# Optimization experiments

Measured on AMD Instinct MI355X. Metric: run time of the kernel, lower is better.

## Reference

```python
import jax, jax.numpy as jnp
import numpy as np
from jax import lax

LEAK = 0.2
GN_EPS = 1e-5
K_NEIGH = 16
GROUPS = 4


def knn_idx(coor_k, coor_q, k):
    # coor_k: [B,Nk,3], coor_q: [B,Nq,3] -> [B,Nq,k] indices of k nearest in coor_k
    d = (jnp.sum(coor_q * coor_q, -1, keepdims=True)
         - 2.0 * jnp.einsum('bqc,bkc->bqk', coor_q, coor_k)
         + jnp.sum(coor_k * coor_k, -1)[:, None, :])
    _, idx = lax.top_k(-d, k)
    return idx


def graph_feature(coor_q, x_q, coor_k, x_k, k):
    # coor_*: [B,3,N*]; x_q: [B,C,Nq]; x_k: [B,C,Nk] -> [B,2C,Nq,k]
    idx = knn_idx(lax.stop_gradient(coor_k).transpose(0, 2, 1),
                  lax.stop_gradient(coor_q).transpose(0, 2, 1), k)
    B = x_k.shape[0]
    x_k_t = x_k.transpose(0, 2, 1)                      # [B,Nk,C]
    b_idx = jnp.arange(B)[:, None, None]
    nb = x_k_t[b_idx, idx]                              # [B,Nq,k,C]
    nb = nb.transpose(0, 3, 1, 2)                       # [B,C,Nq,k]
    xq = x_q[:, :, :, None]                             # [B,C,Nq,1]
    return jnp.concatenate([nb - xq, jnp.broadcast_to(xq, nb.shape)], axis=1)


def conv_gn_lrelu_max(f, w, gamma, beta):
    # f: [B,Cin,N,k]; w: [Cout,Cin] -> [B,Cout,N] (max over k)
    y = jnp.einsum('oc,bcnk->bonk', w, f)
    B, C, N, Kk = y.shape
    g = y.reshape(B, GROUPS, C // GROUPS, N, Kk)
    mu = g.mean((2, 3, 4), keepdims=True)
    var = g.var((2, 3, 4), keepdims=True)
    g = (g - mu) * lax.rsqrt(var + GN_EPS)
    y = g.reshape(B, C, N, Kk) * gamma[None, :, None, None] + beta[None, :, None, None]
    y = jnp.where(y >= 0, y, LEAK * y)
    return y.max(axis=-1)


def fps(xyz, n):
    # xyz: [B,N,3] -> [B,n] int32 (furthest point sampling, start at index 0)
    B, N, _ = xyz.shape
    d0 = jnp.sum((xyz - xyz[:, :1]) ** 2, -1)           # dist to point 0
    def body(dist, _):
        idx = jnp.argmax(dist, -1)                       # [B]
        nxt = jnp.take_along_axis(xyz, idx[:, None, None], 1)
        dist = jnp.minimum(dist, jnp.sum((xyz - nxt) ** 2, -1))
        return dist, idx
    _, idxs = lax.scan(body, d0, None, length=n - 1)     # [n-1,B]
    first = jnp.zeros((1, B), idxs.dtype)
    return jnp.concatenate([first, idxs], 0).T           # [B,n]


def fps_downsample(coor, x, n):
    # coor: [B,3,N], x: [B,C,N] -> ([B,3,n], [B,C,n])
    idx = fps(lax.stop_gradient(coor).transpose(0, 2, 1), n)
    comb = jnp.concatenate([coor, x], axis=1)            # [B,3+C,N]
    b_idx = jnp.arange(coor.shape[0])[:, None]
    new = comb.transpose(0, 2, 1)[b_idx, idx].transpose(0, 2, 1)
    return new[:, :3], new[:, 3:]


def setup_inputs() -> dict:
    key = jax.random.key(0)
    ks = jax.random.split(key, 16)
    s = 0.1
    return {
        'x': jax.random.normal(ks[0], (32, 2048, 3), jnp.float32),
        'w_in': jax.random.normal(ks[1], (8, 3), jnp.float32) * s,
        'b_in': jnp.zeros((8,), jnp.float32),
        'w1': jax.random.normal(ks[2], (32, 16), jnp.float32) * s,
        'g1': jnp.ones((32,), jnp.float32), 'be1': jnp.zeros((32,), jnp.float32),
        'w2': jax.random.normal(ks[3], (64, 64), jnp.float32) * s,
        'g2': jnp.ones((64,), jnp.float32), 'be2': jnp.zeros((64,), jnp.float32),
        'w3': jax.random.normal(ks[4], (64, 128), jnp.float32) * s,
        'g3': jnp.ones((64,), jnp.float32), 'be3': jnp.zeros((64,), jnp.float32),
        'w4': jax.random.normal(ks[5], (256, 128), jnp.float32) * s,
        'g4': jnp.ones((256,), jnp.float32), 'be4': jnp.zeros((256,), jnp.float32),
        'num0': 512,
        'num1': 128,
    }


def reference(x, w_in, b_in, w1, g1, be1, w2, g2, be2, w3, g3, be3, w4, g4, be4, num0, num1):
    coor = x.transpose(0, 2, 1)                          # [B,3,N]
    f = jnp.einsum('oc,bcn->bon', w_in, coor) + b_in[None, :, None]  # input_trans
    f = graph_feature(coor, f, coor, f, K_NEIGH)         # [B,16,N,k]
    f = conv_gn_lrelu_max(f, w1, g1, be1)                # [B,32,N]
    coor_q, f_q = fps_downsample(coor, f, num0)
    f = graph_feature(coor_q, f_q, coor, f, K_NEIGH)     # [B,64,num0,k]
    f = conv_gn_lrelu_max(f, w2, g2, be2)                # [B,64,num0]
    coor = coor_q
    f = graph_feature(coor, f, coor, f, K_NEIGH)         # [B,128,num0,k]
    f = conv_gn_lrelu_max(f, w3, g3, be3)                # [B,64,num0]
    coor_q, f_q = fps_downsample(coor, f, num1)
    f = graph_feature(coor_q, f_q, coor, f, K_NEIGH)     # [B,128,num1,k]
    f = conv_gn_lrelu_max(f, w4, g4, be4)                # [B,256,num1]
    coor = coor_q
    return coor.transpose(0, 2, 1), f.transpose(0, 2, 1)  # [B,num1,3], [B,num1,256]
```

## Files before the change

kernel.cpp:

```cpp
#include <hip/hip_runtime.h>

#define BB 32
#define NPTS0 2048
#define KNB 16
#define KC 256

constexpr int ilog2c(int n){ int l=0; while(n>1){ n>>=1; ++l; } return l; }

static __device__ __forceinline__ float sq3(float a, float b, float c){
  return __fadd_rn(__fadd_rn(__fmul_rn(a,a),__fmul_rn(b,b)),__fmul_rn(c,c));
}

template<int CTRL, int RM>
static __device__ __forceinline__ float dpp_maxf(float v){
  int s = __builtin_amdgcn_update_dpp(__float_as_int(v), __float_as_int(v), CTRL, RM, 0xF, false);
  return fmaxf(v, __int_as_float(s));
}
template<int CTRL, int RM>
static __device__ __forceinline__ unsigned dpp_minu(unsigned v){
  unsigned s = (unsigned)__builtin_amdgcn_update_dpp((int)v, (int)v, CTRL, RM, 0xF, false);
  return s < v ? s : v;
}

static __device__ __forceinline__ void proj_body(const float* __restrict__ x,
    const float* __restrict__ w, const float* __restrict__ bias, float* __restrict__ f0,
    int blk)
{
  int gid = blk*256 + threadIdx.x;
  if (gid >= BB*NPTS0) return;
  float x0 = x[gid*3+0], x1 = x[gid*3+1], x2 = x[gid*3+2];
  #pragma unroll
  for (int o = 0; o < 8; ++o){
    float acc = __fmul_rn(w[o*3+0], x0);
    acc = __fmaf_rn(w[o*3+1], x1, acc);
    acc = __fmaf_rn(w[o*3+2], x2, acc);
    f0[gid*8+o] = __fadd_rn(acc, bias[o]);
  }
}

#define KDECL(I) float th##I = __builtin_inff(); int ti##I = 0;
#define KINS(I,J) if (th##I < th##J){ float tv=th##I; th##I=th##J; th##J=tv; \
                                      int tj=ti##I; ti##I=ti##J; ti##J=tj; }
#define KST(I) pd[base+I] = th##I; pi[base+I] = (unsigned char)ti##I;

static __device__ __forceinline__ void knn_part_body(const float* __restrict__ qpts,
    const float* __restrict__ kpts, int Nq, int Nk, int nkc,
    float* __restrict__ pd, unsigned char* __restrict__ pi,
    int b, int qcb, int kc, float4* kk4)
{
  int tid = threadIdx.x;
  {
    int j = kc*KC + tid;
    float a = kpts[(b*Nk+j)*3+0];
    float c = kpts[(b*Nk+j)*3+1];
    float d = kpts[(b*Nk+j)*3+2];
    kk4[tid] = make_float4(a, c, d, sq3(a,c,d));
  }
  __syncthreads();
  int q = qcb*256 + tid;
  if (q >= Nq) return;
  float qx = qpts[(b*Nq+q)*3+0], qy = qpts[(b*Nq+q)*3+1], qz = qpts[(b*Nq+q)*3+2];
  float qq = sq3(qx,qy,qz);
  KDECL(0) KDECL(1) KDECL(2) KDECL(3) KDECL(4) KDECL(5) KDECL(6) KDECL(7)
  KDECL(8) KDECL(9) KDECL(10) KDECL(11) KDECL(12) KDECL(13) KDECL(14) KDECL(15)
  for (int j=0;j<KC;j++){
    float4 k4 = kk4[j];
    float dot = __fmul_rn(qx,k4.x);
    dot = __fmaf_rn(qy,k4.y,dot);
    dot = __fmaf_rn(qz,k4.z,dot);
    float d = __fadd_rn(__fsub_rn(qq, __fmul_rn(2.0f,dot)), k4.w);
    if (d < th15){
      th15 = d; ti15 = j;
      KINS(15,14) KINS(14,13) KINS(13,12) KINS(12,11) KINS(11,10) KINS(10,9)
      KINS(9,8) KINS(8,7) KINS(7,6) KINS(6,5) KINS(5,4) KINS(4,3) KINS(3,2)
      KINS(2,1) KINS(1,0)
    }
  }
  size_t base = ((size_t)(b*Nq+q)*nkc + kc)*KNB;
  KST(0) KST(1) KST(2) KST(3) KST(4) KST(5) KST(6) KST(7)
  KST(8) KST(9) KST(10) KST(11) KST(12) KST(13) KST(14) KST(15)
}

#define FPS_LOAD(T) float px##T, py##T, pz##T, d##T; { int i_=T*256+tid; \
  px##T=P[i_*3+0]; py##T=P[i_*3+1]; pz##T=P[i_*3+2]; \
  float dx_=__fsub_rn(px##T,c0x), dy_=__fsub_rn(py##T,c0y), dz_=__fsub_rn(pz##T,c0z); \
  d##T=sq3(dx_,dy_,dz_); bm=fmaxf(bm,d##T); }
#define FPS_MATCH(T) if (d##T == m_w) ci = (unsigned)(T*256 + tid);
#define FPS_OWN(T) if ((idx_w>>8) == T##u){ cx=px##T; cy=py##T; cz=pz##T; }
#define FPS_UPD(T) { float dx_=__fsub_rn(px##T,sx), dy_=__fsub_rn(py##T,sy), dz_=__fsub_rn(pz##T,sz); \
  float nd_=sq3(dx_,dy_,dz_); d##T=fminf(d##T,nd_); nbm=fmaxf(nbm,d##T); }

#define FPS_REDUCE_AND_PICK \
    float v = bm; \
    v = dpp_maxf<0x111, 0xF>(v); \
    v = dpp_maxf<0x112, 0xF>(v); \
    v = dpp_maxf<0x114, 0xF>(v); \
    v = dpp_maxf<0x118, 0xF>(v); \
    v = dpp_maxf<0x142, 0xA>(v); \
    v = dpp_maxf<0x143, 0xC>(v); \
    float m_w = __int_as_float(__builtin_amdgcn_readlane(__float_as_int(v), 63)); \
    unsigned ci = 0xFFFFFFFFu;

#define FPS_MIN_AND_MERGE \
    ci = dpp_minu<0x111, 0xF>(ci); \
    ci = dpp_minu<0x112, 0xF>(ci); \
    ci = dpp_minu<0x114, 0xF>(ci); \
    ci = dpp_minu<0x118, 0xF>(ci); \
    ci = dpp_minu<0x142, 0xA>(ci); \
    ci = dpp_minu<0x143, 0xC>(ci); \
    unsigned idx_w = (unsigned)__builtin_amdgcn_readlane((int)ci, 63); \
    int par = s & 1;

#define FPS_CROSSWAVE \
    __syncthreads(); \
    float4 q0 = *(const float4*)&swp[par][0][0]; float z0 = swp[par][0][4]; \
    float4 q1 = *(const float4*)&swp[par][1][0]; float z1 = swp[par][1][4]; \
    float4 q2 = *(const float4*)&swp[par][2][0]; float z2 = swp[par][2][4]; \
    float4 q3 = *(const float4*)&swp[par][3][0]; float z3 = swp[par][3][4]; \
    float mm = q0.x; unsigned mi = __float_as_uint(q0.y); \
    float sx = q0.z, sy = q0.w, sz = z0; \
    if (q1.x > mm || (q1.x == mm && __float_as_uint(q1.y) < mi)){ \
      mm = q1.x; mi = __float_as_uint(q1.y); sx = q1.z; sy = q1.w; sz = z1; } \
    if (q2.x > mm || (q2.x == mm && __float_as_uint(q2.y) < mi)){ \
      mm = q2.x; mi = __float_as_uint(q2.y); sx = q2.z; sy = q2.w; sz = z2; } \
    if (q3.x > mm || (q3.x == mm && __float_as_uint(q3.y) < mi)){ \
      mm = q3.x; mi = __float_as_uint(q3.y); sx = q3.z; sy = q3.w; sz = z3; } \
    if (tid == 0) oibuf[s] = (int)mi;

static __device__ __forceinline__ void fps8_body(const float* __restrict__ pts,
    int S, int* __restrict__ oidx, int b, char* smraw)
{
  float (*swp)[4][8] = reinterpret_cast<float(*)[4][8]>(smraw);
  int* oibuf = reinterpret_cast<int*>(smraw + 256);
  int tid = threadIdx.x, wid = tid >> 6;
  const float* P = pts + (size_t)b*2048*3;
  float c0x = P[0], c0y = P[1], c0z = P[2];
  float bm = -1.0f;
  FPS_LOAD(0) FPS_LOAD(1) FPS_LOAD(2) FPS_LOAD(3)
  FPS_LOAD(4) FPS_LOAD(5) FPS_LOAD(6) FPS_LOAD(7)
  if (tid == 0) oibuf[0] = 0;
  for (int s=1; s<S; ++s){
    FPS_REDUCE_AND_PICK
    FPS_MATCH(7) FPS_MATCH(6) FPS_MATCH(5) FPS_MATCH(4)
    FPS_MATCH(3) FPS_MATCH(2) FPS_MATCH(1) FPS_MATCH(0)
    FPS_MIN_AND_MERGE
    if (tid == (int)(idx_w & 255u)){
      float cx = px0, cy = py0, cz = pz0;
      FPS_OWN(1) FPS_OWN(2) FPS_OWN(3) FPS_OWN(4) FPS_OWN(5) FPS_OWN(6) FPS_OWN(7)
      float4* wp = (float4*)&swp[par][wid][0];
      *wp = make_float4(m_w, __uint_as_float(idx_w), cx, cy);
      swp[par][wid][4] = cz;
    }
    FPS_CROSSWAVE
    float nbm = -1.0f;
    FPS_UPD(0) FPS_UPD(1) FPS_UPD(2) FPS_UPD(3)
    FPS_UPD(4) FPS_UPD(5) FPS_UPD(6) FPS_UPD(7)
    bm = nbm;
  }
  __syncthreads();
  for (int s2 = tid; s2 < S; s2 += 256) oidx[b*S + s2] = oibuf[s2];
}

static __device__ __forceinline__ void fps2_body(const float* __restrict__ pts,
    int S, int* __restrict__ oidx, int b, char* smraw)
{
  float (*swp)[4][8] = reinterpret_cast<float(*)[4][8]>(smraw);
  int* oibuf = reinterpret_cast<int*>(smraw + 256);
  int tid = threadIdx.x, wid = tid >> 6;
  const float* P = pts + (size_t)b*512*3;
  float c0x = P[0], c0y = P[1], c0z = P[2];
  float bm = -1.0f;
  FPS_LOAD(0) FPS_LOAD(1)
  if (tid == 0) oibuf[0] = 0;
  for (int s=1; s<S; ++s){
    FPS_REDUCE_AND_PICK
    FPS_MATCH(1) FPS_MATCH(0)
    FPS_MIN_AND_MERGE
    if (tid == (int)(idx_w & 255u)){
      float cx = px0, cy = py0, cz = pz0;
      FPS_OWN(1)
      float4* wp = (float4*)&swp[par][wid][0];
      *wp = make_float4(m_w, __uint_as_float(idx_w), cx, cy);
      swp[par][wid][4] = cz;
    }
    FPS_CROSSWAVE
    float nbm = -1.0f;
    FPS_UPD(0) FPS_UPD(1)
    bm = nbm;
  }
  __syncthreads();
  for (int s2 = tid; s2 < S; s2 += 256) oidx[b*S + s2] = oibuf[s2];
}

__global__ __launch_bounds__(256) void fused1_kernel(const float* __restrict__ x,
    const float* __restrict__ w_in, const float* __restrict__ b_in,
    float* __restrict__ f0, float* __restrict__ pd1, unsigned char* __restrict__ pi1,
    int* __restrict__ fidx0)
{
  __shared__ __align__(16) char sm[4096];
  int bid = blockIdx.x;
  if (bid < 32){
    __builtin_amdgcn_s_setprio(3);
    fps8_body(x, 512, fidx0, bid, sm);
  } else if (bid < 32+2048){
    int r = bid - 32;
    int b = r & 31; int rest = r >> 5;
    knn_part_body(x, x, 2048, 2048, 8, pd1, pi1, b, rest & 7, rest >> 3, (float4*)sm);
  } else {
    proj_body(x, w_in, b_in, f0, bid - 2080);
  }
}

__global__ __launch_bounds__(256) void fused2_kernel(const float* __restrict__ coorq1,
    const float* __restrict__ x,
    float* __restrict__ pd2, unsigned char* __restrict__ pi2,
    float* __restrict__ pd3, unsigned char* __restrict__ pi3,
    int* __restrict__ fidx1)
{
  __shared__ __align__(16) char sm[4096];
  int bid = blockIdx.x;
  if (bid < 32){
    __builtin_amdgcn_s_setprio(3);
    fps2_body(coorq1, 128, fidx1, bid, sm);
  } else if (bid < 32+512){
    int r = bid - 32;
    int b = r & 31; int rest = r >> 5;
    knn_part_body(coorq1, x, 512, 2048, 8, pd2, pi2, b, rest & 1, rest >> 1, (float4*)sm);
  } else {
    int r = bid - 544;
    int b = r & 31; int rest = r >> 5;
    knn_part_body(coorq1, coorq1, 512, 512, 2, pd3, pi3, b, rest & 1, rest >> 1, (float4*)sm);
  }
}

__global__ __launch_bounds__(256) void knn_part_kernel(const float* __restrict__ qpts,
    const float* __restrict__ kpts, int Nq, int Nk,
    float* __restrict__ pd, unsigned char* __restrict__ pi)
{
  __shared__ __align__(16) float4 kk4[KC];
  knn_part_body(qpts, kpts, Nq, Nk, gridDim.z, pd, pi,
                blockIdx.x, blockIdx.y, blockIdx.z, kk4);
}

__global__ __launch_bounds__(256) void knn_merge_kernel(const float* __restrict__ pd,
    const unsigned char* __restrict__ pi, int Nq, int nkc, int* __restrict__ oidx)
{
  int gid = blockIdx.x*256 + threadIdx.x;
  if (gid >= BB*Nq) return;
  float th[KNB]; int ti[KNB];
  #pragma unroll
  for (int i=0;i<KNB;i++){ th[i] = __builtin_inff(); ti[i] = 0; }
  size_t base = (size_t)gid*nkc*KNB;
  for (int kc=0;kc<nkc;kc++){
    size_t cb = base + (size_t)kc*KNB;
    for (int i=0;i<KNB;i++){
      float d = pd[cb+i];
      if (d >= th[KNB-1]) break;
      int j = kc*KC + (int)pi[cb+i];
      th[KNB-1] = d; ti[KNB-1] = j;
      #pragma unroll
      for (int m=KNB-1;m>0;--m){
        if (th[m] < th[m-1]){
          float tv=th[m]; th[m]=th[m-1]; th[m-1]=tv;
          int tj=ti[m]; ti[m]=ti[m-1]; ti[m-1]=tj;
        }
      }
    }
  }
  #pragma unroll
  for (int i=0;i<KNB;i++) oidx[gid*KNB + i] = ti[i];
}

template<int C, int O, bool DIFF>
__global__ __launch_bounds__(256) void gemv_kernel(const float* __restrict__ fin,
    const float* __restrict__ W, float* __restrict__ out, int Npts)
{
  constexpr int NT = O/8;
  constexpr int LNT = ilog2c(NT);
  int gid = blockIdx.x*256 + threadIdx.x;
  if (gid >= BB*Npts*NT) return;
  int tile = gid & (NT-1);
  int pn = gid >> LNT;
  const float* frow = fin + pn*C;
  float f[C];
  #pragma unroll
  for (int c=0;c<C;c++) f[c] = frow[c];
  float acc[8];
  const float* wbase = W + (tile*8)*(2*C);
  #pragma unroll
  for (int oo=0;oo<8;oo++){
    const float* wrow = wbase + oo*(2*C);
    float a = 0.f;
    #pragma unroll
    for (int c=0;c<C;c++){
      float wv = DIFF ? __fsub_rn(wrow[C+c], wrow[c]) : wrow[c];
      a = __fmaf_rn(wv, f[c], a);
    }
    acc[oo] = a;
  }
  float* orow = out + pn*O + tile*8;
  #pragma unroll
  for (int oo=0;oo<8;oo++) orow[oo] = acc[oo];
}

template<int O>
__global__ __launch_bounds__(256) void stats2_kernel(const float* __restrict__ A,
    const float* __restrict__ Bq, const int* __restrict__ idx, int Nq, int Nk,
    double* __restrict__ part)
{
  constexpr int O4 = O/4;
  int b = blockIdx.x, split = blockIdx.y, nsplit = gridDim.y;
  int qlen = Nq / nsplit, q0 = split*qlen;
  int tid = threadIdx.x;
  int pairs = qlen * KNB;
  double s1[4] = {0.0,0.0,0.0,0.0};
  double s2[4] = {0.0,0.0,0.0,0.0};
  for (int p = tid; p < pairs; p += 256){
    int q = q0 + (p >> 4);
    int kk = p & 15;
    int j = idx[(b*Nq+q)*KNB + kk];
    const float* arow = A + (size_t)(b*Nk+j)*O;
    const float* brow = Bq + (size_t)(b*Nq+q)*O;
    #pragma unroll
    for (int g=0; g<4; ++g){
      float cs1 = 0.f, cs2 = 0.f;
      #pragma unroll
      for (int c=0; c<O4; c+=4){
        float4 a4 = *(const float4*)(arow + g*O4 + c);
        float4 b4 = *(const float4*)(brow + g*O4 + c);
        float y0 = a4.x+b4.x, y1 = a4.y+b4.y, y2 = a4.z+b4.z, y3 = a4.w+b4.w;
        cs1 += ((y0+y1)+(y2+y3));
        cs2 = fmaf(y0,y0,cs2); cs2 = fmaf(y1,y1,cs2);
        cs2 = fmaf(y2,y2,cs2); cs2 = fmaf(y3,y3,cs2);
      }
      s1[g] += (double)cs1;
      s2[g] += (double)cs2;
    }
  }
  #pragma unroll
  for (int m=32;m>0;m>>=1){
    #pragma unroll
    for (int g=0; g<4; ++g){
      s1[g] += __shfl_down(s1[g], m);
      s2[g] += __shfl_down(s2[g], m);
    }
  }
  __shared__ double sh[4][8];
  int lane = tid & 63, w = tid >> 6;
  if (lane == 0){
    #pragma unroll
    for (int g=0; g<4; ++g){ sh[w][g*2] = s1[g]; sh[w][g*2+1] = s2[g]; }
  }
  __syncthreads();
  if (tid == 0){
    #pragma unroll
    for (int g=0; g<4; ++g){
      double t1 = (sh[0][g*2]+sh[1][g*2]) + (sh[2][g*2]+sh[3][g*2]);
      double t2 = (sh[0][g*2+1]+sh[1][g*2+1]) + (sh[2][g*2+1]+sh[3][g*2+1]);
      int pi = (b*4+g)*nsplit + split;
      part[pi*2] = t1; part[pi*2+1] = t2;
    }
  }
}

__global__ __launch_bounds__(128) void statsred_kernel(const double* __restrict__ part,
    int nsplit, double cnt, float* __restrict__ stats)
{
  int t = threadIdx.x;
  if (t >= BB*4) return;
  double s1=0.0, s2=0.0;
  for (int i=0;i<nsplit;i++){ s1 += part[(t*nsplit+i)*2]; s2 += part[(t*nsplit+i)*2+1]; }
  double mean = s1/cnt;
  double var = s2/cnt - mean*mean;
  double rstd = 1.0 / sqrt(var + 1e-5);
  stats[t*2] = (float)mean;
  stats[t*2+1] = (float)rstd;
}

template<int O>
__global__ __launch_bounds__(256) void final_kernel(const float* __restrict__ A,
    const float* __restrict__ Bq, const int* __restrict__ idx,
    const float* __restrict__ stats, const float* __restrict__ gamma,
    const float* __restrict__ beta, float* __restrict__ fout, int Nq, int Nk)
{
  constexpr int LO = ilog2c(O);
  constexpr int LO4 = ilog2c(O/4);
  int b = blockIdx.y;
  int t = blockIdx.x*256 + threadIdx.x;
  if (t >= Nq*O) return;
  int o = t & (O-1);
  int q = t >> LO;
  int g = o >> LO4;
  float mu   = stats[(b*4+g)*2];
  float rstd = stats[(b*4+g)*2+1];
  float gam = gamma[o], bet = beta[o];
  float bq = Bq[(b*Nq+q)*O + o];
  const int* ip = idx + (b*Nq+q)*KNB;
  float m = -__builtin_inff();
  #pragma unroll
  for (int kk=0;kk<KNB;kk++){
    int j = ip[kk];
    float y = A[(b*Nk+j)*O + o] + bq;
    float yn = __fmul_rn(__fsub_rn(y, mu), rstd);
    float yv = __fadd_rn(__fmul_rn(yn, gam), bet);
    float l = yv >= 0.f ? yv : 0.2f*yv;
    m = fmaxf(m, l);
  }
  fout[(b*Nq+q)*O + o] = m;
}

template<int C>
__global__ __launch_bounds__(256) void gather_kernel(const int* __restrict__ fidx,
    const float* __restrict__ pts, const float* __restrict__ fin,
    float* __restrict__ cq, float* __restrict__ fq, int Nin, int Nout)
{
  int gid = blockIdx.x*256 + threadIdx.x;
  if (gid >= BB*Nout) return;
  int b = gid / Nout;
  int i = gid - b*Nout;
  int src = fidx[b*Nout + i];
  #pragma unroll
  for (int c=0;c<3;c++) cq[gid*3+c] = pts[(b*Nin+src)*3+c];
  #pragma unroll
  for (int c=0;c<C;c++) fq[gid*C+c] = fin[(b*Nin+src)*C+c];
}

__global__ __launch_bounds__(256) void gatherc_kernel(const int* __restrict__ fidx,
    const float* __restrict__ pts, float* __restrict__ cq, int Nin, int Nout)
{
  int gid = blockIdx.x*256 + threadIdx.x;
  if (gid >= BB*Nout) return;
  int b = gid / Nout;
  int i = gid - b*Nout;
  int src = fidx[b*Nout + i];
  #pragma unroll
  for (int c=0;c<3;c++) cq[gid*3+c] = pts[(b*Nin+src)*3+c];
}

template<int C>
__global__ __launch_bounds__(256) void gatherf_kernel(const int* __restrict__ fidx,
    const float* __restrict__ fin, float* __restrict__ fq, int Nin, int Nout)
{
  int gid = blockIdx.x*256 + threadIdx.x;
  if (gid >= BB*Nout) return;
  int b = gid / Nout;
  int i = gid - b*Nout;
  int src = fidx[b*Nout + i];
  #pragma unroll
  for (int c=0;c<C;c++) fq[gid*C+c] = fin[(b*Nin+src)*C+c];
}

extern "C" void kernel_launch(void* const* d_in, const int* in_sizes, int n_in,
                              void* d_out, int out_size, void* d_ws, size_t ws_size,
                              hipStream_t stream)
{
  (void)in_sizes; (void)n_in; (void)out_size; (void)ws_size;
  const float* x    = (const float*)d_in[0];
  const float* w_in = (const float*)d_in[1];
  const float* b_in = (const float*)d_in[2];
  const float* w1 = (const float*)d_in[3];
  const float* g1 = (const float*)d_in[4];
  const float* be1= (const float*)d_in[5];
  const float* w2 = (const float*)d_in[6];
  const float* g2 = (const float*)d_in[7];
  const float* be2= (const float*)d_in[8];
  const float* w3 = (const float*)d_in[9];
  const float* g3 = (const float*)d_in[10];
  const float* be3= (const float*)d_in[11];
  const float* w4 = (const float*)d_in[12];
  const float* g4 = (const float*)d_in[13];
  const float* be4= (const float*)d_in[14];

  float* out = (float*)d_out;
  float* coor_out = out;
  float* f_out = out + BB*128*3;

  char* ws = (char*)d_ws;
  size_t off = 0;
  auto alloc = [&](size_t bytes)->void*{ void* p = ws + off; off += (bytes + 255) & ~(size_t)255; return p; };

  float* f0     = (float*)alloc((size_t)BB*2048*8*4);
  int*   idx1   = (int*)  alloc((size_t)BB*2048*16*4);
  float* f1     = (float*)alloc((size_t)BB*2048*32*4);
  double* part  = (double*)alloc((size_t)BB*4*8*2*8);
  float* statsv = (float*)alloc((size_t)BB*4*2*4);
  int*   fidx0  = (int*)  alloc((size_t)BB*512*4);
  float* coorq1 = (float*)alloc((size_t)BB*512*3*4);
  float* fq1    = (float*)alloc((size_t)BB*512*32*4);
  int*   idx2   = (int*)  alloc((size_t)BB*512*16*4);
  float* f2     = (float*)alloc((size_t)BB*512*64*4);
  int*   idx3   = (int*)  alloc((size_t)BB*512*16*4);
  float* f3     = (float*)alloc((size_t)BB*512*64*4);
  int*   fidx1  = (int*)  alloc((size_t)BB*128*4);
  float* fq2    = (float*)alloc((size_t)BB*128*64*4);
  int*   idx4   = (int*)  alloc((size_t)BB*128*16*4);
  float* pd2          = (float*)alloc((size_t)BB*512*8*KNB*4);
  unsigned char* pi2  = (unsigned char*)alloc((size_t)BB*512*8*KNB);
  float* pd3          = (float*)alloc((size_t)BB*512*2*KNB*4);
  unsigned char* pi3  = (unsigned char*)alloc((size_t)BB*512*2*KNB);
  float* pd4          = (float*)alloc((size_t)BB*128*2*KNB*4);
  unsigned char* pi4  = (unsigned char*)alloc((size_t)BB*128*2*KNB);

  char* U = (char*)alloc((size_t)48<<20);
  float* pd1         = (float*)U;
  unsigned char* pi1 = (unsigned char*)(U + ((size_t)34<<20));
  float* A  = (float*)U;
  float* Bq = (float*)(U + ((size_t)20<<20));

  auto cdiv = [](int a, int b){ return (a+b-1)/b; };

  fused1_kernel<<<2336,256,0,stream>>>(x, w_in, b_in, f0, pd1, pi1, fidx0);

  knn_merge_kernel<<<cdiv(BB*2048,256),256,0,stream>>>(pd1, pi1, 2048, 8, idx1);
  gemv_kernel<8,32,false><<<cdiv(BB*2048*4,256),256,0,stream>>>(f0, w1, A, 2048);
  gemv_kernel<8,32,true ><<<cdiv(BB*2048*4,256),256,0,stream>>>(f0, w1, Bq, 2048);
  stats2_kernel<32><<<dim3(BB,8),256,0,stream>>>(A, Bq, idx1, 2048, 2048, part);
  statsred_kernel<<<1,128,0,stream>>>(part, 8, 8.0*2048*16, statsv);
  final_kernel<32><<<dim3(cdiv(2048*32,256),BB),256,0,stream>>>(A, Bq, idx1, statsv, g1, be1, f1, 2048, 2048);

  gather_kernel<32><<<cdiv(BB*512,256),256,0,stream>>>(fidx0, x, f1, coorq1, fq1, 2048, 512);

  fused2_kernel<<<672,256,0,stream>>>(coorq1, x, pd2, pi2, pd3, pi3, fidx1);

  knn_merge_kernel<<<cdiv(BB*512,256),256,0,stream>>>(pd2, pi2, 512, 8, idx2);
  knn_merge_kernel<<<cdiv(BB*512,256),256,0,stream>>>(pd3, pi3, 512, 2, idx3);

  gatherc_kernel<<<cdiv(BB*128,256),256,0,stream>>>(fidx1, coorq1, coor_out, 512, 128);
  knn_part_kernel<<<dim3(BB,1,2),256,0,stream>>>(coor_out, coorq1, 128, 512, pd4, pi4);
  knn_merge_kernel<<<cdiv(BB*128,256),256,0,stream>>>(pd4, pi4, 128, 2, idx4);

  gemv_kernel<32,64,false><<<cdiv(BB*2048*8,256),256,0,stream>>>(f1, w2, A, 2048);
  gemv_kernel<32,64,true ><<<cdiv(BB*512*8,256),256,0,stream>>>(fq1, w2, Bq, 512);
  stats2_kernel<64><<<dim3(BB,8),256,0,stream>>>(A, Bq, idx2, 512, 2048, part);
  statsred_kernel<<<1,128,0,stream>>>(part, 8, 16.0*512*16, statsv);
  final_kernel<64><<<dim3(cdiv(512*64,256),BB),256,0,stream>>>(A, Bq, idx2, statsv, g2, be2, f2, 512, 2048);

  gemv_kernel<64,64,false><<<cdiv(BB*512*8,256),256,0,stream>>>(f2, w3, A, 512);
  gemv_kernel<64,64,true ><<<cdiv(BB*512*8,256),256,0,stream>>>(f2, w3, Bq, 512);
  stats2_kernel<64><<<dim3(BB,8),256,0,stream>>>(A, Bq, idx3, 512, 512, part);
  statsred_kernel<<<1,128,0,stream>>>(part, 8, 16.0*512*16, statsv);
  final_kernel<64><<<dim3(cdiv(512*64,256),BB),256,0,stream>>>(A, Bq, idx3, statsv, g3, be3, f3, 512, 512);

  gatherf_kernel<64><<<cdiv(BB*128,256),256,0,stream>>>(fidx1, f3, fq2, 512, 128);
  gemv_kernel<64,256,false><<<cdiv(BB*512*32,256),256,0,stream>>>(f3, w4, A, 512);
  gemv_kernel<64,256,true ><<<cdiv(BB*128*32,256),256,0,stream>>>(fq2, w4, Bq, 128);
  stats2_kernel<256><<<dim3(BB,8),256,0,stream>>>(A, Bq, idx4, 128, 512, part);
  statsred_kernel<<<1,128,0,stream>>>(part, 8, 64.0*128*16, statsv);
  final_kernel<256><<<dim3(cdiv(128*256,256),BB),256,0,stream>>>(A, Bq, idx4, statsv, g4, be4, f_out, 128, 512);
}
```

Baseline: 1.364 ms.

## Pack FPS distance and index into 64-bit key for single-pass argmax reduction

The furthest point sampling loop now packs the distance bits and inverted point index into a 64-bit key. A single DPP max chain then yields both the maximum and its lowest index, replacing the separate max reduction, match and min-index reduction passes. Point coordinates are staged in shared memory so every thread reads the selected centre directly, removing the owner-thread writeback of coordinates. The cost is larger shared-memory allocations in the fused kernels (about 34 KB), which may lower occupancy for the co-scheduled kNN and projection blocks, plus 64-bit compares in the update loop.

```diff
diff --git a/kernel.cpp b/kernel.cpp
--- a/kernel.cpp
+++ b/kernel.cpp
@@ -12,14 +12,12 @@
 }
 
 template<int CTRL, int RM>
-static __device__ __forceinline__ float dpp_maxf(float v){
-  int s = __builtin_amdgcn_update_dpp(__float_as_int(v), __float_as_int(v), CTRL, RM, 0xF, false);
-  return fmaxf(v, __int_as_float(s));
-}
-template<int CTRL, int RM>
-static __device__ __forceinline__ unsigned dpp_minu(unsigned v){
-  unsigned s = (unsigned)__builtin_amdgcn_update_dpp((int)v, (int)v, CTRL, RM, 0xF, false);
-  return s < v ? s : v;
+static __device__ __forceinline__ void dppmax64(unsigned &blo, unsigned &bhi){
+  unsigned slo = (unsigned)__builtin_amdgcn_update_dpp((int)blo, (int)blo, CTRL, RM, 0xF, true);
+  unsigned shi = (unsigned)__builtin_amdgcn_update_dpp((int)bhi, (int)bhi, CTRL, RM, 0xF, true);
+  unsigned long long a = ((unsigned long long)bhi<<32) | blo;
+  unsigned long long q = ((unsigned long long)shi<<32) | slo;
+  if (q > a){ blo = slo; bhi = shi; }
 }
 
 static __device__ __forceinline__ void proj_body(const float* __restrict__ x,
@@ -81,81 +79,61 @@
   KST(8) KST(9) KST(10) KST(11) KST(12) KST(13) KST(14) KST(15)
 }
 
-#define FPS_LOAD(T) float px##T, py##T, pz##T, d##T; { int i_=T*256+tid; \
+#define FQ_LOAD(T) float px##T, py##T, pz##T, d##T; { int i_=T*256+tid; \
   px##T=P[i_*3+0]; py##T=P[i_*3+1]; pz##T=P[i_*3+2]; \
+  p4[i_] = make_float4(px##T, py##T, pz##T, 0.f); \
   float dx_=__fsub_rn(px##T,c0x), dy_=__fsub_rn(py##T,c0y), dz_=__fsub_rn(pz##T,c0z); \
-  d##T=sq3(dx_,dy_,dz_); bm=fmaxf(bm,d##T); }
-#define FPS_MATCH(T) if (d##T == m_w) ci = (unsigned)(T*256 + tid);
-#define FPS_OWN(T) if ((idx_w>>8) == T##u){ cx=px##T; cy=py##T; cz=pz##T; }
-#define FPS_UPD(T) { float dx_=__fsub_rn(px##T,sx), dy_=__fsub_rn(py##T,sy), dz_=__fsub_rn(pz##T,sz); \
-  float nd_=sq3(dx_,dy_,dz_); d##T=fminf(d##T,nd_); nbm=fmaxf(nbm,d##T); }
-
-#define FPS_REDUCE_AND_PICK \
-    float v = bm; \
-    v = dpp_maxf<0x111, 0xF>(v); \
-    v = dpp_maxf<0x112, 0xF>(v); \
-    v = dpp_maxf<0x114, 0xF>(v); \
-    v = dpp_maxf<0x118, 0xF>(v); \
-    v = dpp_maxf<0x142, 0xA>(v); \
-    v = dpp_maxf<0x143, 0xC>(v); \
-    float m_w = __int_as_float(__builtin_amdgcn_readlane(__float_as_int(v), 63)); \
-    unsigned ci = 0xFFFFFFFFu;
-
-#define FPS_MIN_AND_MERGE \
-    ci = dpp_minu<0x111, 0xF>(ci); \
-    ci = dpp_minu<0x112, 0xF>(ci); \
-    ci = dpp_minu<0x114, 0xF>(ci); \
-    ci = dpp_minu<0x118, 0xF>(ci); \
-    ci = dpp_minu<0x142, 0xA>(ci); \
-    ci = dpp_minu<0x143, 0xC>(ci); \
-    unsigned idx_w = (unsigned)__builtin_amdgcn_readlane((int)ci, 63); \
-    int par = s & 1;
-
-#define FPS_CROSSWAVE \
-    __syncthreads(); \
-    float4 q0 = *(const float4*)&swp[par][0][0]; float z0 = swp[par][0][4]; \
-    float4 q1 = *(const float4*)&swp[par][1][0]; float z1 = swp[par][1][4]; \
-    float4 q2 = *(const float4*)&swp[par][2][0]; float z2 = swp[par][2][4]; \
-    float4 q3 = *(const float4*)&swp[par][3][0]; float z3 = swp[par][3][4]; \
-    float mm = q0.x; unsigned mi = __float_as_uint(q0.y); \
-    float sx = q0.z, sy = q0.w, sz = z0; \
-    if (q1.x > mm || (q1.x == mm && __float_as_uint(q1.y) < mi)){ \
-      mm = q1.x; mi = __float_as_uint(q1.y); sx = q1.z; sy = q1.w; sz = z1; } \
-    if (q2.x > mm || (q2.x == mm && __float_as_uint(q2.y) < mi)){ \
-      mm = q2.x; mi = __float_as_uint(q2.y); sx = q2.z; sy = q2.w; sz = z2; } \
-    if (q3.x > mm || (q3.x == mm && __float_as_uint(q3.y) < mi)){ \
-      mm = q3.x; mi = __float_as_uint(q3.y); sx = q3.z; sy = q3.w; sz = z3; } \
-    if (tid == 0) oibuf[s] = (int)mi;
+  d##T=sq3(dx_,dy_,dz_); \
+  unsigned long long k_=((unsigned long long)__float_as_uint(d##T)<<32)|~(unsigned)i_; \
+  if (k_ > bk) bk = k_; }
+#define FQ_UPD(T) { float dx_=__fsub_rn(px##T,sx), dy_=__fsub_rn(py##T,sy), dz_=__fsub_rn(pz##T,sz); \
+  float nd_=sq3(dx_,dy_,dz_); d##T=fminf(d##T,nd_); \
+  unsigned long long k_=((unsigned long long)__float_as_uint(d##T)<<32)|~(unsigned)(T*256+tid); \
+  if (k_ > bk) bk = k_; }
+
+#define FQ_CHAIN \
+    unsigned blo = (unsigned)bk, bhi = (unsigned)(bk>>32); \
+    dppmax64<0x111,0xF>(blo,bhi); \
+    dppmax64<0x112,0xF>(blo,bhi); \
+    dppmax64<0x114,0xF>(blo,bhi); \
+    dppmax64<0x118,0xF>(blo,bhi); \
+    dppmax64<0x142,0xA>(blo,bhi); \
+    dppmax64<0x143,0xC>(blo,bhi); \
+    int par = s & 1; \
+    if ((tid & 63) == 63) swk[par*4 + wid] = ((unsigned long long)bhi<<32) | blo; \
+    __syncthreads();
+
+#define FQ_MERGE \
+    unsigned long long k0 = swk[par*4+0], k1 = swk[par*4+1]; \
+    unsigned long long k2 = swk[par*4+2], k3 = swk[par*4+3]; \
+    if (k1 > k0) k0 = k1; \
+    if (k3 > k2) k2 = k3; \
+    if (k2 > k0) k0 = k2; \
+    int fi = (int)(~(unsigned)k0); \
+    if (tid == 0) oibuf[s] = fi; \
+    float4 cs = p4[fi]; \
+    float sx = cs.x, sy = cs.y, sz = cs.z;
 
 static __device__ __forceinline__ void fps8_body(const float* __restrict__ pts,
     int S, int* __restrict__ oidx, int b, char* smraw)
 {
-  float (*swp)[4][8] = reinterpret_cast<float(*)[4][8]>(smraw);
-  int* oibuf = reinterpret_cast<int*>(smraw + 256);
+  float4* p4 = (float4*)smraw;
+  unsigned long long* swk = (unsigned long long*)(smraw + 32768);
+  int* oibuf = (int*)(smraw + 32768 + 64);
   int tid = threadIdx.x, wid = tid >> 6;
   const float* P = pts + (size_t)b*2048*3;
   float c0x = P[0], c0y = P[1], c0z = P[2];
-  float bm = -1.0f;
-  FPS_LOAD(0) FPS_LOAD(1) FPS_LOAD(2) FPS_LOAD(3)
-  FPS_LOAD(4) FPS_LOAD(5) FPS_LOAD(6) FPS_LOAD(7)
+  unsigned long long bk = 0ull;
+  FQ_LOAD(0) FQ_LOAD(1) FQ_LOAD(2) FQ_LOAD(3)
+  FQ_LOAD(4) FQ_LOAD(5) FQ_LOAD(6) FQ_LOAD(7)
   if (tid == 0) oibuf[0] = 0;
+  __syncthreads();
   for (int s=1; s<S; ++s){
-    FPS_REDUCE_AND_PICK
-    FPS_MATCH(7) FPS_MATCH(6) FPS_MATCH(5) FPS_MATCH(4)
-    FPS_MATCH(3) FPS_MATCH(2) FPS_MATCH(1) FPS_MATCH(0)
-    FPS_MIN_AND_MERGE
-    if (tid == (int)(idx_w & 255u)){
-      float cx = px0, cy = py0, cz = pz0;
-      FPS_OWN(1) FPS_OWN(2) FPS_OWN(3) FPS_OWN(4) FPS_OWN(5) FPS_OWN(6) FPS_OWN(7)
-      float4* wp = (float4*)&swp[par][wid][0];
-      *wp = make_float4(m_w, __uint_as_float(idx_w), cx, cy);
-      swp[par][wid][4] = cz;
-    }
-    FPS_CROSSWAVE
-    float nbm = -1.0f;
-    FPS_UPD(0) FPS_UPD(1) FPS_UPD(2) FPS_UPD(3)
-    FPS_UPD(4) FPS_UPD(5) FPS_UPD(6) FPS_UPD(7)
-    bm = nbm;
+    FQ_CHAIN
+    FQ_MERGE
+    bk = 0ull;
+    FQ_UPD(0) FQ_UPD(1) FQ_UPD(2) FQ_UPD(3)
+    FQ_UPD(4) FQ_UPD(5) FQ_UPD(6) FQ_UPD(7)
   }
   __syncthreads();
   for (int s2 = tid; s2 < S; s2 += 256) oidx[b*S + s2] = oibuf[s2];
@@ -164,29 +142,21 @@
 static __device__ __forceinline__ void fps2_body(const float* __restrict__ pts,
     int S, int* __restrict__ oidx, int b, char* smraw)
 {
-  float (*swp)[4][8] = reinterpret_cast<float(*)[4][8]>(smraw);
-  int* oibuf = reinterpret_cast<int*>(smraw + 256);
+  float4* p4 = (float4*)smraw;
+  unsigned long long* swk = (unsigned long long*)(smraw + 8192);
+  int* oibuf = (int*)(smraw + 8192 + 64);
   int tid = threadIdx.x, wid = tid >> 6;
   const float* P = pts + (size_t)b*512*3;
   float c0x = P[0], c0y = P[1], c0z = P[2];
-  float bm = -1.0f;
-  FPS_LOAD(0) FPS_LOAD(1)
+  unsigned long long bk = 0ull;
+  FQ_LOAD(0) FQ_LOAD(1)
   if (tid == 0) oibuf[0] = 0;
+  __syncthreads();
   for (int s=1; s<S; ++s){
-    FPS_REDUCE_AND_PICK
-    FPS_MATCH(1) FPS_MATCH(0)
-    FPS_MIN_AND_MERGE
-    if (tid == (int)(idx_w & 255u)){
-      float cx = px0, cy = py0, cz = pz0;
-      FPS_OWN(1)
-      float4* wp = (float4*)&swp[par][wid][0];
-      *wp = make_float4(m_w, __uint_as_float(idx_w), cx, cy);
-      swp[par][wid][4] = cz;
-    }
-    FPS_CROSSWAVE
-    float nbm = -1.0f;
-    FPS_UPD(0) FPS_UPD(1)
-    bm = nbm;
+    FQ_CHAIN
+    FQ_MERGE
+    bk = 0ull;
+    FQ_UPD(0) FQ_UPD(1)
   }
   __syncthreads();
   for (int s2 = tid; s2 < S; s2 += 256) oidx[b*S + s2] = oibuf[s2];
@@ -197,7 +167,7 @@
     float* __restrict__ f0, float* __restrict__ pd1, unsigned char* __restrict__ pi1,
     int* __restrict__ fidx0)
 {
-  __shared__ __align__(16) char sm[4096];
+  __shared__ __align__(16) char sm[34880];
   int bid = blockIdx.x;
   if (bid < 32){
     __builtin_amdgcn_s_setprio(3);
@@ -217,7 +187,7 @@
     float* __restrict__ pd3, unsigned char* __restrict__ pi3,
     int* __restrict__ fidx1)
 {
-  __shared__ __align__(16) char sm[4096];
+  __shared__ __align__(16) char sm[8768];
   int bid = blockIdx.x;
   if (bid < 32){
     __builtin_amdgcn_s_setprio(3);
```

Result: no change. 1.371 ms (+0.5%).

## Fuse launches: merge A/B gemvs, fold statsred into final, overlap knn merge with fused2

Applied to the files above, without the earlier changes.

Several kernel launches are merged to cut launch overhead and idle gaps. The A and B gemv projections now run in one dual kernel. The group-norm stats reduction moves into final_kernel, so each block reduces its batch's partials. The first-stage kNN merge runs as extra blocks of fused2_kernel, which overlaps it with FPS and the later kNN partials, and coordinate gathering is split out ahead of it. This adds redundant per-block stats reduction and makes fused2's work more uneven across blocks.

```diff
diff --git a/kernel.cpp b/kernel.cpp
--- a/kernel.cpp
+++ b/kernel.cpp
@@ -41,7 +41,11 @@
 #define KDECL(I) float th##I = __builtin_inff(); int ti##I = 0;
 #define KINS(I,J) if (th##I < th##J){ float tv=th##I; th##I=th##J; th##J=tv; \
                                       int tj=ti##I; ti##I=ti##J; ti##J=tj; }
+#define KCASCADE KINS(15,14) KINS(14,13) KINS(13,12) KINS(12,11) KINS(11,10) \
+  KINS(10,9) KINS(9,8) KINS(8,7) KINS(7,6) KINS(6,5) KINS(5,4) KINS(4,3) \
+  KINS(3,2) KINS(2,1) KINS(1,0)
 #define KST(I) pd[base+I] = th##I; pi[base+I] = (unsigned char)ti##I;
+#define MST(I) oidx[obase+I] = ti##I;
 
 static __device__ __forceinline__ void knn_part_body(const float* __restrict__ qpts,
     const float* __restrict__ kpts, int Nq, int Nk, int nkc,
@@ -71,14 +75,36 @@
     float d = __fadd_rn(__fsub_rn(qq, __fmul_rn(2.0f,dot)), k4.w);
     if (d < th15){
       th15 = d; ti15 = j;
-      KINS(15,14) KINS(14,13) KINS(13,12) KINS(12,11) KINS(11,10) KINS(10,9)
-      KINS(9,8) KINS(8,7) KINS(7,6) KINS(6,5) KINS(5,4) KINS(4,3) KINS(3,2)
-      KINS(2,1) KINS(1,0)
+      KCASCADE
     }
   }
   size_t base = ((size_t)(b*Nq+q)*nkc + kc)*KNB;
   KST(0) KST(1) KST(2) KST(3) KST(4) KST(5) KST(6) KST(7)
   KST(8) KST(9) KST(10) KST(11) KST(12) KST(13) KST(14) KST(15)
+}
+
+static __device__ __forceinline__ void knn_merge_body(const float* __restrict__ pd,
+    const unsigned char* __restrict__ pi, int Nq, int nkc, int* __restrict__ oidx,
+    int blk)
+{
+  int gid = blk*256 + threadIdx.x;
+  if (gid >= BB*Nq) return;
+  KDECL(0) KDECL(1) KDECL(2) KDECL(3) KDECL(4) KDECL(5) KDECL(6) KDECL(7)
+  KDECL(8) KDECL(9) KDECL(10) KDECL(11) KDECL(12) KDECL(13) KDECL(14) KDECL(15)
+  size_t base = (size_t)gid*nkc*KNB;
+  for (int kc=0;kc<nkc;kc++){
+    size_t cb = base + (size_t)kc*KNB;
+    for (int i=0;i<KNB;i++){
+      float d = pd[cb+i];
+      if (d >= th15) break;
+      int j = kc*KC + (int)pi[cb+i];
+      th15 = d; ti15 = j;
+      KCASCADE
+    }
+  }
+  int obase = gid*KNB;
+  MST(0) MST(1) MST(2) MST(3) MST(4) MST(5) MST(6) MST(7)
+  MST(8) MST(9) MST(10) MST(11) MST(12) MST(13) MST(14) MST(15)
 }
 
 #define FPS_LOAD(T) float px##T, py##T, pz##T, d##T; { int i_=T*256+tid; \
@@ -215,7 +241,9 @@
     const float* __restrict__ x,
     float* __restrict__ pd2, unsigned char* __restrict__ pi2,
     float* __restrict__ pd3, unsigned char* __restrict__ pi3,
-    int* __restrict__ fidx1)
+    int* __restrict__ fidx1,
+    const float* __restrict__ pd1, const unsigned char* __restrict__ pi1,
+    int* __restrict__ idx1)
 {
   __shared__ __align__(16) char sm[4096];
   int bid = blockIdx.x;
@@ -226,10 +254,12 @@
     int r = bid - 32;
     int b = r & 31; int rest = r >> 5;
     knn_part_body(coorq1, x, 512, 2048, 8, pd2, pi2, b, rest & 1, rest >> 1, (float4*)sm);
-  } else {
+  } else if (bid < 32+512+128){
     int r = bid - 544;
     int b = r & 31; int rest = r >> 5;
     knn_part_body(coorq1, coorq1, 512, 512, 2, pd3, pi3, b, rest & 1, rest >> 1, (float4*)sm);
+  } else {
+    knn_merge_body(pd1, pi1, 2048, 8, idx1, bid - 672);
   }
 }
 
@@ -245,39 +275,16 @@
 __global__ __launch_bounds__(256) void knn_merge_kernel(const float* __restrict__ pd,
     const unsigned char* __restrict__ pi, int Nq, int nkc, int* __restrict__ oidx)
 {
-  int gid = blockIdx.x*256 + threadIdx.x;
-  if (gid >= BB*Nq) return;
-  float th[KNB]; int ti[KNB];
-  #pragma unroll
-  for (int i=0;i<KNB;i++){ th[i] = __builtin_inff(); ti[i] = 0; }
-  size_t base = (size_t)gid*nkc*KNB;
-  for (int kc=0;kc<nkc;kc++){
-    size_t cb = base + (size_t)kc*KNB;
-    for (int i=0;i<KNB;i++){
-      float d = pd[cb+i];
-      if (d >= th[KNB-1]) break;
-      int j = kc*KC + (int)pi[cb+i];
-      th[KNB-1] = d; ti[KNB-1] = j;
-      #pragma unroll
-      for (int m=KNB-1;m>0;--m){
-        if (th[m] < th[m-1]){
-          float tv=th[m]; th[m]=th[m-1]; th[m-1]=tv;
-          int tj=ti[m]; ti[m]=ti[m-1]; ti[m-1]=tj;
-        }
-      }
-    }
-  }
-  #pragma unroll
-  for (int i=0;i<KNB;i++) oidx[gid*KNB + i] = ti[i];
+  knn_merge_body(pd, pi, Nq, nkc, oidx, blockIdx.x);
 }
 
 template<int C, int O, bool DIFF>
-__global__ __launch_bounds__(256) void gemv_kernel(const float* __restrict__ fin,
-    const float* __restrict__ W, float* __restrict__ out, int Npts)
+static __device__ __forceinline__ void gemv_body(const float* __restrict__ fin,
+    const float* __restrict__ W, float* __restrict__ out, int Npts, int blk)
 {
   constexpr int NT = O/8;
   constexpr int LNT = ilog2c(NT);
-  int gid = blockIdx.x*256 + threadIdx.x;
+  int gid = blk*256 + threadIdx.x;
   if (gid >= BB*Npts*NT) return;
   int tile = gid & (NT-1);
   int pn = gid >> LNT;
@@ -301,6 +308,17 @@
   float* orow = out + pn*O + tile*8;
   #pragma unroll
   for (int oo=0;oo<8;oo++) orow[oo] = acc[oo];
+}
+
+template<int C, int O>
+__global__ __launch_bounds__(256) void gemv_dual_kernel(const float* __restrict__ finA,
+    const float* __restrict__ finB, const float* __restrict__ W,
+    float* __restrict__ outA, float* __restrict__ outB,
+    int NptsA, int NptsB, int nAblk)
+{
+  int bid = blockIdx.x;
+  if (bid < nAblk) gemv_body<C,O,false>(finA, W, outA, NptsA, bid);
+  else             gemv_body<C,O,true >(finB, W, outB, NptsB, bid - nAblk);
 }
 
 template<int O>
@@ -363,36 +381,36 @@
   }
 }
 
-__global__ __launch_bounds__(128) void statsred_kernel(const double* __restrict__ part,
-    int nsplit, double cnt, float* __restrict__ stats)
-{
-  int t = threadIdx.x;
-  if (t >= BB*4) return;
-  double s1=0.0, s2=0.0;
-  for (int i=0;i<nsplit;i++){ s1 += part[(t*nsplit+i)*2]; s2 += part[(t*nsplit+i)*2+1]; }
-  double mean = s1/cnt;
-  double var = s2/cnt - mean*mean;
-  double rstd = 1.0 / sqrt(var + 1e-5);
-  stats[t*2] = (float)mean;
-  stats[t*2+1] = (float)rstd;
-}
-
 template<int O>
 __global__ __launch_bounds__(256) void final_kernel(const float* __restrict__ A,
     const float* __restrict__ Bq, const int* __restrict__ idx,
-    const float* __restrict__ stats, const float* __restrict__ gamma,
-    const float* __restrict__ beta, float* __restrict__ fout, int Nq, int Nk)
+    const double* __restrict__ part, int nsplit, double cnt,
+    const float* __restrict__ gamma, const float* __restrict__ beta,
+    float* __restrict__ fout, int Nq, int Nk)
 {
   constexpr int LO = ilog2c(O);
   constexpr int LO4 = ilog2c(O/4);
+  __shared__ float smu[4], srs[4];
   int b = blockIdx.y;
+  if (threadIdx.x < 4){
+    int g = threadIdx.x;
+    int t0 = b*4+g;
+    double s1=0.0, s2=0.0;
+    for (int i=0;i<nsplit;i++){ s1 += part[(t0*nsplit+i)*2]; s2 += part[(t0*nsplit+i)*2+1]; }
+    double mean = s1/cnt;
+    double var = s2/cnt - mean*mean;
+    double rstd = 1.0 / sqrt(var + 1e-5);
+    smu[g] = (float)mean;
+    srs[g] = (float)rstd;
+  }
+  __syncthreads();
   int t = blockIdx.x*256 + threadIdx.x;
   if (t >= Nq*O) return;
   int o = t & (O-1);
   int q = t >> LO;
   int g = o >> LO4;
-  float mu   = stats[(b*4+g)*2];
-  float rstd = stats[(b*4+g)*2+1];
+  float mu   = smu[g];
+  float rstd = srs[g];
   float gam = gamma[o], bet = beta[o];
   float bq = Bq[(b*Nq+q)*O + o];
   const int* ip = idx + (b*Nq+q)*KNB;
@@ -407,22 +425,6 @@
     m = fmaxf(m, l);
   }
   fout[(b*Nq+q)*O + o] = m;
-}
-
-template<int C>
-__global__ __launch_bounds__(256) void gather_kernel(const int* __restrict__ fidx,
-    const float* __restrict__ pts, const float* __restrict__ fin,
-    float* __restrict__ cq, float* __restrict__ fq, int Nin, int Nout)
-{
-  int gid = blockIdx.x*256 + threadIdx.x;
-  if (gid >= BB*Nout) return;
-  int b = gid / Nout;
-  int i = gid - b*Nout;
-  int src = fidx[b*Nout + i];
-  #pragma unroll
-  for (int c=0;c<3;c++) cq[gid*3+c] = pts[(b*Nin+src)*3+c];
-  #pragma unroll
-  for (int c=0;c<C;c++) fq[gid*C+c] = fin[(b*Nin+src)*C+c];
 }
 
 __global__ __launch_bounds__(256) void gatherc_kernel(const int* __restrict__ fidx,
@@ -483,7 +485,6 @@
   int*   idx1   = (int*)  alloc((size_t)BB*2048*16*4);
   float* f1     = (float*)alloc((size_t)BB*2048*32*4);
   double* part  = (double*)alloc((size_t)BB*4*8*2*8);
-  float* statsv = (float*)alloc((size_t)BB*4*2*4);
   int*   fidx0  = (int*)  alloc((size_t)BB*512*4);
   float* coorq1 = (float*)alloc((size_t)BB*512*3*4);
   float* fq1    = (float*)alloc((size_t)BB*512*32*4);
@@ -511,16 +512,16 @@
 
   fused1_kernel<<<2336,256,0,stream>>>(x, w_in, b_in, f0, pd1, pi1, fidx0);
 
-  knn_merge_kernel<<<cdiv(BB*2048,256),256,0,stream>>>(pd1, pi1, 2048, 8, idx1);
-  gemv_kernel<8,32,false><<<cdiv(BB*2048*4,256),256,0,stream>>>(f0, w1, A, 2048);
-  gemv_kernel<8,32,true ><<<cdiv(BB*2048*4,256),256,0,stream>>>(f0, w1, Bq, 2048);
+  gatherc_kernel<<<cdiv(BB*512,256),256,0,stream>>>(fidx0, x, coorq1, 2048, 512);
+
+  fused2_kernel<<<928,256,0,stream>>>(coorq1, x, pd2, pi2, pd3, pi3, fidx1,
+                                      pd1, pi1, idx1);
+
+  gemv_dual_kernel<8,32><<<2048,256,0,stream>>>(f0, f0, w1, A, Bq, 2048, 2048, 1024);
   stats2_kernel<32><<<dim3(BB,8),256,0,stream>>>(A, Bq, idx1, 2048, 2048, part);
-  statsred_kernel<<<1,128,0,stream>>>(part, 8, 8.0*2048*16, statsv);
-  final_kernel<32><<<dim3(cdiv(2048*32,256),BB),256,0,stream>>>(A, Bq, idx1, statsv, g1, be1, f1, 2048, 2048);
-
-  gather_kernel<32><<<cdiv(BB*512,256),256,0,stream>>>(fidx0, x, f1, coorq1, fq1, 2048, 512);
-
-  fused2_kernel<<<672,256,0,stream>>>(coorq1, x, pd2, pi2, pd3, pi3, fidx1);
+  final_kernel<32><<<dim3(cdiv(2048*32,256),BB),256,0,stream>>>(A, Bq, idx1, part, 8,
+      8.0*2048*16, g1, be1, f1, 2048, 2048);
+  gatherf_kernel<32><<<cdiv(BB*512,256),256,0,stream>>>(fidx0, f1, fq1, 2048, 512);
 
   knn_merge_kernel<<<cdiv(BB*512,256),256,0,stream>>>(pd2, pi2, 512, 8, idx2);
   knn_merge_kernel<<<cdiv(BB*512,256),256,0,stream>>>(pd3, pi3, 512, 2, idx3);
@@ -529,22 +530,19 @@
   knn_part_kernel<<<dim3(BB,1,2),256,0,stream>>>(coor_out, coorq1, 128, 512, pd4, pi4);
   knn_merge_kernel<<<cdiv(BB*128,256),256,0,stream>>>(pd4, pi4, 128, 2, idx4);
 
-  gemv_kernel<32,64,false><<<cdiv(BB*2048*8,256),256,0,stream>>>(f1, w2, A, 2048);
-  gemv_kernel<32,64,true ><<<cdiv(BB*512*8,256),256,0,stream>>>(fq1, w2, Bq, 512);
+  gemv_dual_kernel<32,64><<<2560,256,0,stream>>>(f1, fq1, w2, A, Bq, 2048, 512, 2048);
   stats2_kernel<64><<<dim3(BB,8),256,0,stream>>>(A, Bq, idx2, 512, 2048, part);
-  statsred_kernel<<<1,128,0,stream>>>(part, 8, 16.0*512*16, statsv);
-  final_kernel<64><<<dim3(cdiv(512*64,256),BB),256,0,stream>>>(A, Bq, idx2, statsv, g2, be2, f2, 512, 2048);
-
-  gemv_kernel<64,64,false><<<cdiv(BB*512*8,256),256,0,stream>>>(f2, w3, A, 512);
-  gemv_kernel<64,64,true ><<<cdiv(BB*512*8,256),256,0,stream>>>(f2, w3, Bq, 512);
+  final_kernel<64><<<dim3(cdiv(512*64,256),BB),256,0,stream>>>(A, Bq, idx2, part, 8,
+      16.0*512*16, g2, be2, f2, 512, 2048);
+
+  gemv_dual_kernel<64,64><<<1024,256,0,stream>>>(f2, f2, w3, A, Bq, 512, 512, 512);
   stats2_kernel<64><<<dim3(BB,8),256,0,stream>>>(A, Bq, idx3, 512, 512, part);
-  statsred_kernel<<<1,128,0,stream>>>(part, 8, 16.0*512*16, statsv);
-  final_kernel<64><<<dim3(cdiv(512*64,256),BB),256,0,stream>>>(A, Bq, idx3, statsv, g3, be3, f3, 512, 512);
+  final_kernel<64><<<dim3(cdiv(512*64,256),BB),256,0,stream>>>(A, Bq, idx3, part, 8,
+      16.0*512*16, g3, be3, f3, 512, 512);
 
   gatherf_kernel<64><<<cdiv(BB*128,256),256,0,stream>>>(fidx1, f3, fq2, 512, 128);
-  gemv_kernel<64,256,false><<<cdiv(BB*512*32,256),256,0,stream>>>(f3, w4, A, 512);
-  gemv_kernel<64,256,true ><<<cdiv(BB*128*32,256),256,0,stream>>>(fq2, w4, Bq, 128);
+  gemv_dual_kernel<64,256><<<2560,256,0,stream>>>(f3, fq2, w4, A, Bq, 512, 128, 2048);
   stats2_kernel<256><<<dim3(BB,8),256,0,stream>>>(A, Bq, idx4, 128, 512, part);
-  statsred_kernel<<<1,128,0,stream>>>(part, 8, 64.0*128*16, statsv);
-  final_kernel<256><<<dim3(cdiv(128*256,256),BB),256,0,stream>>>(A, Bq, idx4, statsv, g4, be4, f_out, 128, 512);
-}
+  final_kernel<256><<<dim3(cdiv(128*256,256),BB),256,0,stream>>>(A, Bq, idx4, part, 8,
+      64.0*128*16, g4, be4, f_out, 128, 512);
+}
```

Result: faster. 1.337 ms (-2.0%).
